# Kernel optimization log

Measured on AMD Instinct MI355X. Metric: run time of the kernel, lower is better.

The kernel has to match this reference:

```python
import jax, jax.numpy as jnp
import numpy as np

B, C_IN, C_OUT, N, K = 1, 64, 64, 50000, 20


def setup_inputs() -> dict:
    key = jax.random.key(0)
    k1, k2, k3, k4, k5 = jax.random.split(key, 5)
    x = jax.random.normal(k1, (B, C_IN, N, 1), dtype=jnp.float32)
    edge_index = jax.random.randint(k2, (2, B, N, K), 0, N, dtype=jnp.int64)
    dis = jax.random.uniform(k3, (B, N, K), dtype=jnp.float32)
    W = jax.random.normal(k4, (C_OUT, 2 * C_IN), dtype=jnp.float32) * (2.0 / (2 * C_IN)) ** 0.5
    b = jnp.zeros((C_OUT,), dtype=jnp.float32)
    att_w = jax.random.normal(k5, (K,), dtype=jnp.float32) * (2.0 / K) ** 0.5
    att_b = jnp.zeros((1,), dtype=jnp.float32)
    return {"x": x, "edge_index": edge_index, "dis": dis, "W": W, "b": b,
            "att_w": att_w, "att_b": att_b}


def reference(x, edge_index, dis, W, b, att_w, att_b):
    # x: [B, C, N, 1]; edge_index: [2, B, N, K]; dis: [B, N, K]
    x2 = x[..., 0]  # [B, C, N]
    gather = jax.vmap(lambda xb, ib: xb[:, ib])  # per-batch: [C,N] idx[N,K] -> [C,N,K]
    x_i = gather(x2, edge_index[1])  # [B, C, N, K]
    x_j = gather(x2, edge_index[0])  # [B, C, N, K]
    feat = jnp.concatenate([x_i, x_j - x_i], axis=1)  # [B, 2C, N, K]
    # 1x1 conv == channel contraction
    feat = jax.nn.relu(jnp.einsum('oc,bcnk->bonk', W, feat) + b[None, :, None, None])
    # attention over the k channel of dis -> per-node scaler
    scaler = jnp.tanh(jnp.einsum('k,bnk->bn', att_w, dis) + att_b) + 1.0  # [B, N]
    suppression = 2.0 * jax.nn.sigmoid(-dis * scaler[:, :, None])  # [B, N, K]
    feat = feat * suppression[:, None, :, :]  # [B, C_out, N, K]
    return jnp.max(feat, axis=-1, keepdims=True)  # [B, C_out, N, 1]
```

## Files before the change

kernel.cpp:

```cpp
#include <hip/hip_runtime.h>
#include <hip/hip_bf16.h>

#define NN 50000
#define CC 64
#define KK 20

static __device__ __forceinline__ ushort f2bf(float f) {
    unsigned int u = __float_as_uint(f);
    unsigned int r = (u + 0x7FFFu + ((u >> 16) & 1u)) >> 16;
    return (ushort)r;
}
static __device__ __forceinline__ float bfl(unsigned int u) {
    return __uint_as_float(u << 16);
}
static __device__ __forceinline__ float bfh(unsigned int u) {
    return __uint_as_float(u & 0xffff0000u);
}

__global__ __launch_bounds__(256) void prep_kernel(
    const float* __restrict__ x,
    const float* __restrict__ W,
    const float* __restrict__ b,
    ushort* __restrict__ yA,
    ushort* __restrict__ yB)
{
    __shared__ float At[64][65];
    __shared__ float Bt[64][65];
    __shared__ float xt[64][68];

    const int t = threadIdx.x;
    for (int i = t; i < 64 * 64; i += 256) {
        int c = i >> 6, ci = i & 63;
        float w1 = W[c * 128 + ci];
        float w2 = W[c * 128 + 64 + ci];
        At[ci][c] = w1 - w2;
        Bt[ci][c] = w2;
    }

    const int n0 = blockIdx.x * 64;
    const int g  = t >> 6;
    const int nl = t & 63;
    #pragma unroll
    for (int i = 0; i < 16; i++) {
        int ci = i * 4 + g;
        int nn = n0 + nl;
        xt[ci][nl] = (nn < NN) ? x[ci * NN + nn] : 0.f;
    }
    __syncthreads();

    const int c = t & 63;
    float accA[16], accB[16];
    #pragma unroll
    for (int j = 0; j < 16; j++) { accA[j] = 0.f; accB[j] = 0.f; }

    for (int ci = 0; ci < 64; ci++) {
        float a  = At[ci][c];
        float w2 = Bt[ci][c];
        const float4* xr = reinterpret_cast<const float4*>(&xt[ci][g * 16]);
        #pragma unroll
        for (int q = 0; q < 4; q++) {
            float4 xv = xr[q];
            accA[q * 4 + 0] += a * xv.x;  accB[q * 4 + 0] += w2 * xv.x;
            accA[q * 4 + 1] += a * xv.y;  accB[q * 4 + 1] += w2 * xv.y;
            accA[q * 4 + 2] += a * xv.z;  accB[q * 4 + 2] += w2 * xv.z;
            accA[q * 4 + 3] += a * xv.w;  accB[q * 4 + 3] += w2 * xv.w;
        }
    }

    float bias = b[c];
    #pragma unroll
    for (int j = 0; j < 16; j++) {
        int n = n0 + g * 16 + j;
        if (n < NN) {
            yA[n * 64 + c] = f2bf(accA[j] + bias);
            yB[n * 64 + c] = f2bf(accB[j]);
        }
    }
}

__global__ __launch_bounds__(256) void edge_kernel(
    const ushort* __restrict__ yA,
    const ushort* __restrict__ yB,
    const int* __restrict__ ej,
    const int* __restrict__ ei,
    const float* __restrict__ dis,
    const float* __restrict__ att_w,
    const float* __restrict__ att_b,
    float* __restrict__ out)
{
    __shared__ float tile[16][68];

    const int t    = threadIdx.x;
    const int lane = t & 63;
    const int w    = t >> 6;
    const int g    = lane >> 4;
    const int l    = lane & 15;
    const int n0   = blockIdx.x * 16;
    const int nb   = n0 + w * 4;

    const float aw = (lane < KK) ? att_w[lane] : 0.f;
    const float ab = att_b[0];

    float d4[4]; int ii4[4], jj4[4];
    #pragma unroll
    for (int s = 0; s < 4; s++) {
        const int n = nb + s;
        float d = 0.f; int ii = 0, jj = 0;
        if (lane < KK) {
            d  = dis[n * KK + lane];
            ii = ei[n * KK + lane];
            jj = ej[n * KK + lane];
        }
        d4[s] = d; ii4[s] = ii; jj4[s] = jj;
    }

    float sup4[4];
    #pragma unroll
    for (int s = 0; s < 4; s++) {
        float p = aw * d4[s];
        #pragma unroll
        for (int off = 16; off > 0; off >>= 1) p += __shfl_down(p, off);
        const float scaler = tanhf(__shfl(p, 0) + ab) + 1.0f;
        sup4[s] = 2.0f / (1.0f + __expf(d4[s] * scaler));
    }

    const uint2* A2 = (const uint2*)yA;
    const uint2* B2 = (const uint2*)yB;

    #pragma unroll
    for (int s = 0; s < 4; s++) {
        float4 m = {0.f, 0.f, 0.f, 0.f};
        #pragma unroll
        for (int kb = 0; kb < 5; kb++) {
            const int   src = kb * 4 + g;
            const int   i_k = __shfl(ii4[s], src);
            const int   j_k = __shfl(jj4[s], src);
            const float sp  = __shfl(sup4[s], src);
            const uint2 a = A2[(size_t)i_k * 16 + l];
            const uint2 bb = B2[(size_t)j_k * 16 + l];
            float v;
            v = fmaxf(bfl(a.x) + bfl(bb.x), 0.f) * sp;  m.x = fmaxf(m.x, v);
            v = fmaxf(bfh(a.x) + bfh(bb.x), 0.f) * sp;  m.y = fmaxf(m.y, v);
            v = fmaxf(bfl(a.y) + bfl(bb.y), 0.f) * sp;  m.z = fmaxf(m.z, v);
            v = fmaxf(bfh(a.y) + bfh(bb.y), 0.f) * sp;  m.w = fmaxf(m.w, v);
        }
        #pragma unroll
        for (int mask = 16; mask <= 32; mask <<= 1) {
            m.x = fmaxf(m.x, __shfl_xor(m.x, mask));
            m.y = fmaxf(m.y, __shfl_xor(m.y, mask));
            m.z = fmaxf(m.z, __shfl_xor(m.z, mask));
            m.w = fmaxf(m.w, __shfl_xor(m.w, mask));
        }
        if (g == 0) *(float4*)&tile[w * 4 + s][l * 4] = m;
    }
    __syncthreads();

    #pragma unroll
    for (int it = 0; it < 4; it++) {
        const int c  = it * 16 + (t >> 4);
        const int nl = t & 15;
        out[(size_t)c * NN + n0 + nl] = tile[nl][c];
    }
}

extern "C" void kernel_launch(void* const* d_in, const int* in_sizes, int n_in,
                              void* d_out, int out_size, void* d_ws, size_t ws_size,
                              hipStream_t stream) {
    const float* x     = (const float*)d_in[0];
    const int*   e     = (const int*)d_in[1];
    const float* dis   = (const float*)d_in[2];
    const float* W     = (const float*)d_in[3];
    const float* b     = (const float*)d_in[4];
    const float* att_w = (const float*)d_in[5];
    const float* att_b = (const float*)d_in[6];
    float* out = (float*)d_out;

    ushort* yA = (ushort*)d_ws;
    ushort* yB = yA + (size_t)NN * 64;

    prep_kernel<<<(NN + 63) / 64, 256, 0, stream>>>(x, W, b, yA, yB);
    edge_kernel<<<NN / 16, 256, 0, stream>>>(yA, yB, e, e + NN * KK, dis,
                                             att_w, att_b, out);
}
```

Measured before the change: 133.8 us.

## Widen edge gathers to 16-byte loads and prefetch next node's neighbors

The edge kernel now has each lane load a uint4 (8 bf16 channels), so 8 lanes cover one 64-channel row and 8 neighbors are handled per pass, in 3 passes instead of 5. Lanes beyond neighbor 19 in the last pass are clamped to neighbor 19; the duplicate value does not change the max. Gathers for the next node are issued into a double-buffered register set before the current node is reduced, to overlap gather latency with compute. The cost is more registers, one extra cross-lane max-reduction step, and some redundant loads from the clamped lanes.

```diff
diff --git a/kernel.cpp b/kernel.cpp
--- a/kernel.cpp
+++ b/kernel.cpp
@@ -93,10 +93,9 @@
     const int t    = threadIdx.x;
     const int lane = t & 63;
     const int w    = t >> 6;
-    const int g    = lane >> 4;
-    const int l    = lane & 15;
+    const int g    = lane >> 3;
+    const int l    = lane & 7;
     const int n0   = blockIdx.x * 16;
-    const int nb   = n0 + w * 4;
 
     const float aw = (lane < KK) ? att_w[lane] : 0.f;
     const float ab = att_b[0];
@@ -104,7 +103,7 @@
     float d4[4]; int ii4[4], jj4[4];
     #pragma unroll
     for (int s = 0; s < 4; s++) {
-        const int n = nb + s;
+        const int n = n0 + w * 4 + s;
         float d = 0.f; int ii = 0, jj = 0;
         if (lane < KK) {
             d  = dis[n * KK + lane];
@@ -113,7 +112,6 @@
         }
         d4[s] = d; ii4[s] = ii; jj4[s] = jj;
     }
-
     float sup4[4];
     #pragma unroll
     for (int s = 0; s < 4; s++) {
@@ -124,35 +122,76 @@
         sup4[s] = 2.0f / (1.0f + __expf(d4[s] * scaler));
     }
 
-    const uint2* A2 = (const uint2*)yA;
-    const uint2* B2 = (const uint2*)yB;
+    const uint4* A4 = (const uint4*)yA;
+    const uint4* B4 = (const uint4*)yB;
+
+    const int src0 = (0 * 8 + g);
+    const int src1 = (1 * 8 + g);
+    const int src2 = (2 * 8 + g) > 19 ? 19 : (16 + g);
+
+    uint4 av[2][3], bv[2][3];
+
+    #define ISSUE(s, buf)                                                     \
+        {                                                                     \
+            const int i0 = __shfl(ii4[s], src0), j0 = __shfl(jj4[s], src0);   \
+            const int i1 = __shfl(ii4[s], src1), j1 = __shfl(jj4[s], src1);   \
+            const int i2 = __shfl(ii4[s], src2), j2 = __shfl(jj4[s], src2);   \
+            av[buf][0] = A4[(size_t)i0 * 8 + l];                              \
+            bv[buf][0] = B4[(size_t)j0 * 8 + l];                              \
+            av[buf][1] = A4[(size_t)i1 * 8 + l];                              \
+            bv[buf][1] = B4[(size_t)j1 * 8 + l];                              \
+            av[buf][2] = A4[(size_t)i2 * 8 + l];                              \
+            bv[buf][2] = B4[(size_t)j2 * 8 + l];                              \
+        }
+
+    ISSUE(0, 0)
 
     #pragma unroll
     for (int s = 0; s < 4; s++) {
-        float4 m = {0.f, 0.f, 0.f, 0.f};
-        #pragma unroll
-        for (int kb = 0; kb < 5; kb++) {
-            const int   src = kb * 4 + g;
-            const int   i_k = __shfl(ii4[s], src);
-            const int   j_k = __shfl(jj4[s], src);
-            const float sp  = __shfl(sup4[s], src);
-            const uint2 a = A2[(size_t)i_k * 16 + l];
-            const uint2 bb = B2[(size_t)j_k * 16 + l];
-            float v;
-            v = fmaxf(bfl(a.x) + bfl(bb.x), 0.f) * sp;  m.x = fmaxf(m.x, v);
-            v = fmaxf(bfh(a.x) + bfh(bb.x), 0.f) * sp;  m.y = fmaxf(m.y, v);
-            v = fmaxf(bfl(a.y) + bfl(bb.y), 0.f) * sp;  m.z = fmaxf(m.z, v);
-            v = fmaxf(bfh(a.y) + bfh(bb.y), 0.f) * sp;  m.w = fmaxf(m.w, v);
-        }
-        #pragma unroll
-        for (int mask = 16; mask <= 32; mask <<= 1) {
-            m.x = fmaxf(m.x, __shfl_xor(m.x, mask));
-            m.y = fmaxf(m.y, __shfl_xor(m.y, mask));
-            m.z = fmaxf(m.z, __shfl_xor(m.z, mask));
-            m.w = fmaxf(m.w, __shfl_xor(m.w, mask));
-        }
-        if (g == 0) *(float4*)&tile[w * 4 + s][l * 4] = m;
-    }
+        if (s < 3) {
+            if (s == 0) ISSUE(1, 1)
+            if (s == 1) ISSUE(2, 0)
+            if (s == 2) ISSUE(3, 1)
+        }
+        const int buf = s & 1;
+        const float sp0 = __shfl(sup4[s], src0);
+        const float sp1 = __shfl(sup4[s], src1);
+        const float sp2 = __shfl(sup4[s], src2);
+
+        float m[8];
+        #pragma unroll
+        for (int c = 0; c < 8; c++) m[c] = 0.f;
+
+        #pragma unroll
+        for (int kb = 0; kb < 3; kb++) {
+            const float s_k = (kb == 0) ? sp0 : (kb == 1) ? sp1 : sp2;
+            const uint4 a = av[buf][kb];
+            const uint4 bb = bv[buf][kb];
+            m[0] = fmaxf(m[0], (bfl(a.x) + bfl(bb.x)) * s_k);
+            m[1] = fmaxf(m[1], (bfh(a.x) + bfh(bb.x)) * s_k);
+            m[2] = fmaxf(m[2], (bfl(a.y) + bfl(bb.y)) * s_k);
+            m[3] = fmaxf(m[3], (bfh(a.y) + bfh(bb.y)) * s_k);
+            m[4] = fmaxf(m[4], (bfl(a.z) + bfl(bb.z)) * s_k);
+            m[5] = fmaxf(m[5], (bfh(a.z) + bfh(bb.z)) * s_k);
+            m[6] = fmaxf(m[6], (bfl(a.w) + bfl(bb.w)) * s_k);
+            m[7] = fmaxf(m[7], (bfh(a.w) + bfh(bb.w)) * s_k);
+        }
+
+        #pragma unroll
+        for (int mask = 8; mask <= 32; mask <<= 1) {
+            #pragma unroll
+            for (int c = 0; c < 8; c++) m[c] = fmaxf(m[c], __shfl_xor(m[c], mask));
+        }
+
+        if (g == 0) {
+            const int nl = w * 4 + s;
+            float4 lo = {m[0], m[1], m[2], m[3]};
+            float4 hi = {m[4], m[5], m[6], m[7]};
+            *(float4*)&tile[nl][l * 8]     = lo;
+            *(float4*)&tile[nl][l * 8 + 4] = hi;
+        }
+    }
+    #undef ISSUE
     __syncthreads();
 
     #pragma unroll
```

Measured after the change: 137.3 us. +2.6%, slower.

## Retile prep kernel to 128 nodes per block with 2 channels per thread

Applied to the files above, without the earlier changes.

The projection prep kernel now handles 128 nodes per block, loads x with float4 vector reads, and has each thread compute two output channels for 16 nodes. It then writes packed pairs of bf16 as 32-bit stores. The aim is to make global loads and stores wider and to reuse each x value from shared memory across more channels. The cost is more accumulator registers per thread and half as many blocks. The edge kernel is unchanged apart from whitespace.

```diff
diff --git a/kernel.cpp b/kernel.cpp
--- a/kernel.cpp
+++ b/kernel.cpp
@@ -24,9 +24,9 @@
     ushort* __restrict__ yA,
     ushort* __restrict__ yB)
 {
-    __shared__ float At[64][65];
-    __shared__ float Bt[64][65];
-    __shared__ float xt[64][68];
+    __shared__ float At[64][66];
+    __shared__ float Bt[64][66];
+    __shared__ float xt[64][132];
 
     const int t = threadIdx.x;
     for (int i = t; i < 64 * 64; i += 256) {
@@ -37,43 +37,58 @@
         Bt[ci][c] = w2;
     }
 
-    const int n0 = blockIdx.x * 64;
-    const int g  = t >> 6;
-    const int nl = t & 63;
-    #pragma unroll
-    for (int i = 0; i < 16; i++) {
-        int ci = i * 4 + g;
-        int nn = n0 + nl;
-        xt[ci][nl] = (nn < NN) ? x[ci * NN + nn] : 0.f;
+    const int n0 = blockIdx.x * 128;
+    {
+        const int q  = t & 31;
+        const int cb = t >> 5;
+        const float4* x4 = (const float4*)x;
+        const int nq = (n0 >> 2) + q;
+        #pragma unroll
+        for (int i = 0; i < 8; i++) {
+            const int ci = cb * 8 + i;
+            float4 v = (nq < 12500) ? x4[ci * 12500 + nq]
+                                    : float4{0.f, 0.f, 0.f, 0.f};
+            *(float4*)&xt[ci][q * 4] = v;
+        }
     }
     __syncthreads();
 
-    const int c = t & 63;
-    float accA[16], accB[16];
+    const int c2 = t & 31;
+    const int g  = t >> 5;
+
+    float aA0[16], aA1[16], aB0[16], aB1[16];
     #pragma unroll
-    for (int j = 0; j < 16; j++) { accA[j] = 0.f; accB[j] = 0.f; }
+    for (int j = 0; j < 16; j++) { aA0[j]=0.f; aA1[j]=0.f; aB0[j]=0.f; aB1[j]=0.f; }
 
     for (int ci = 0; ci < 64; ci++) {
-        float a  = At[ci][c];
-        float w2 = Bt[ci][c];
-        const float4* xr = reinterpret_cast<const float4*>(&xt[ci][g * 16]);
+        const float2 a  = *(const float2*)&At[ci][c2 * 2];
+        const float2 w2 = *(const float2*)&Bt[ci][c2 * 2];
+        const float4* xr = (const float4*)&xt[ci][g * 16];
         #pragma unroll
         for (int q = 0; q < 4; q++) {
             float4 xv = xr[q];
-            accA[q * 4 + 0] += a * xv.x;  accB[q * 4 + 0] += w2 * xv.x;
-            accA[q * 4 + 1] += a * xv.y;  accB[q * 4 + 1] += w2 * xv.y;
-            accA[q * 4 + 2] += a * xv.z;  accB[q * 4 + 2] += w2 * xv.z;
-            accA[q * 4 + 3] += a * xv.w;  accB[q * 4 + 3] += w2 * xv.w;
+            aA0[q*4+0] += a.x*xv.x;  aA1[q*4+0] += a.y*xv.x;
+            aB0[q*4+0] += w2.x*xv.x; aB1[q*4+0] += w2.y*xv.x;
+            aA0[q*4+1] += a.x*xv.y;  aA1[q*4+1] += a.y*xv.y;
+            aB0[q*4+1] += w2.x*xv.y; aB1[q*4+1] += w2.y*xv.y;
+            aA0[q*4+2] += a.x*xv.z;  aA1[q*4+2] += a.y*xv.z;
+            aB0[q*4+2] += w2.x*xv.z; aB1[q*4+2] += w2.y*xv.z;
+            aA0[q*4+3] += a.x*xv.w;  aA1[q*4+3] += a.y*xv.w;
+            aB0[q*4+3] += w2.x*xv.w; aB1[q*4+3] += w2.y*xv.w;
         }
     }
 
-    float bias = b[c];
+    const float b0 = b[c2 * 2], b1 = b[c2 * 2 + 1];
+    unsigned int* yA32 = (unsigned int*)yA;
+    unsigned int* yB32 = (unsigned int*)yB;
     #pragma unroll
     for (int j = 0; j < 16; j++) {
-        int n = n0 + g * 16 + j;
+        const int n = n0 + g * 16 + j;
         if (n < NN) {
-            yA[n * 64 + c] = f2bf(accA[j] + bias);
-            yB[n * 64 + c] = f2bf(accB[j]);
+            yA32[n * 32 + c2] = (unsigned int)f2bf(aA0[j] + b0)
+                              | ((unsigned int)f2bf(aA1[j] + b1) << 16);
+            yB32[n * 32 + c2] = (unsigned int)f2bf(aB0[j])
+                              | ((unsigned int)f2bf(aB1[j]) << 16);
         }
     }
 }
@@ -136,7 +151,7 @@
             const int   i_k = __shfl(ii4[s], src);
             const int   j_k = __shfl(jj4[s], src);
             const float sp  = __shfl(sup4[s], src);
-            const uint2 a = A2[(size_t)i_k * 16 + l];
+            const uint2 a  = A2[(size_t)i_k * 16 + l];
             const uint2 bb = B2[(size_t)j_k * 16 + l];
             float v;
             v = fmaxf(bfl(a.x) + bfl(bb.x), 0.f) * sp;  m.x = fmaxf(m.x, v);
@@ -178,7 +193,7 @@
     ushort* yA = (ushort*)d_ws;
     ushort* yB = yA + (size_t)NN * 64;
 
-    prep_kernel<<<(NN + 63) / 64, 256, 0, stream>>>(x, W, b, yA, yB);
+    prep_kernel<<<(NN + 127) / 128, 256, 0, stream>>>(x, W, b, yA, yB);
     edge_kernel<<<NN / 16, 256, 0, stream>>>(yA, yB, e, e + NN * KK, dis,
                                              att_w, att_b, out);
 }
```

Result: faster. 127.4 us (-4.8%).
